# Optimization experiments

Hardware: AMD Instinct MI355X
Metric: run time of the kernel (lower is better)

## Reference

```python
import jax, jax.numpy as jnp
import numpy as np

B, T, H, S = 64, 512, 768, 128  # batch, seq_len, hidden_size, num_statements


def setup_inputs() -> dict:
    key = jax.random.key(0)
    ks = jax.random.split(key, 6)
    hidden = jax.random.normal(ks[0], (B, T, H), dtype=jnp.float32)
    # per-token statement ids, sorted (statements appear contiguously in source order)
    statements_ids = jnp.sort(jax.random.randint(ks[1], (B, T), 0, S), axis=-1).astype(jnp.int32)
    scale = 1.0 / np.sqrt(H)
    w1 = jax.random.normal(ks[2], (H, H), dtype=jnp.float32) * scale
    b1 = jnp.zeros((H,), dtype=jnp.float32)
    w2 = jax.random.normal(ks[3], (H, H), dtype=jnp.float32) * scale
    b2 = jnp.zeros((H,), dtype=jnp.float32)
    w3 = jax.random.normal(ks[4], (H, 1), dtype=jnp.float32) * scale
    b3 = jnp.zeros((1,), dtype=jnp.float32)
    return {"hidden": hidden, "statements_ids": statements_ids,
            "w1": w1, "b1": b1, "w2": w2, "b2": b2, "w3": w3, "b3": b3}


def _segment_mean(x, sid):
    # x: [T, H], sid: [T] -> [S, H] mean of tokens per statement id
    sums = jax.ops.segment_sum(x, sid, num_segments=S)            # [S, H]
    cnts = jax.ops.segment_sum(jnp.ones((x.shape[0],), x.dtype), sid, num_segments=S)  # [S]
    return sums / jnp.maximum(cnts, 1.0)[:, None]


def reference(hidden, statements_ids, w1, b1, w2, b2, w3, b3):
    # per-statement mean pooling (scatter-mean), vectorized over batch
    pooled = jax.vmap(_segment_mean)(hidden, statements_ids)      # [B, S, H]
    # CodeCoverageMLP: fc1 -> GELU -> fc2 -> GELU -> fc3 -> sigmoid (dropout = eval identity)
    x = jax.nn.gelu(pooled @ w1 + b1, approximate=False)
    x = jax.nn.gelu(x @ w2 + b2, approximate=False)
    preds = jax.nn.sigmoid(x @ w3 + b3)                           # [B, S, 1]
    return preds[..., 0]                                          # [B, S]
```

## Files before the change

### kernel.cpp

```cpp
#include <hip/hip_runtime.h>
#include <stdint.h>

#define NB 64
#define NT 512
#define NH 768
#define NS 128
#define NM (NB*NS)

typedef _Float16 half8 __attribute__((ext_vector_type(8)));
typedef _Float16 half4 __attribute__((ext_vector_type(4)));
typedef __attribute__((ext_vector_type(4))) float f32x4;

__device__ __forceinline__ float gelu_exact(float x) {
  return 0.5f * x * (1.0f + erff(x * 0.70710678118654752440f));
}

__device__ __forceinline__ void gll16(const void* g, void* l) {
  __builtin_amdgcn_global_load_lds(
      (__attribute__((address_space(1))) unsigned int*)g,
      (__attribute__((address_space(3))) unsigned int*)l,
      16, 0, 0);
}

__global__ void prep_w_kernel(const float* __restrict__ w1, const float* __restrict__ w2,
                              _Float16* __restrict__ W) {
  int id = blockIdx.x * 256 + threadIdx.x;
  int n  = id % NH;
  int t  = id / NH;
  int kc = t % 96;
  int w  = t / 96;
  const float* src = w ? w2 : w1;
  int k0 = kc * 8;
  half8 h;
#pragma unroll
  for (int i = 0; i < 8; ++i)
    h[i] = (_Float16)src[(size_t)(k0 + i) * NH + n];
  const size_t off = ((((size_t)w * 48 + (n >> 4)) * 96 + kc) * 16 + (n & 15)) * 8;
  *(half8*)&W[off] = h;
}

__global__ __launch_bounds__(256)
void pool_kernel(const float* __restrict__ hidden, const int* __restrict__ sid,
                 _Float16* __restrict__ Ahi, _Float16* __restrict__ Alo) {
  __shared__ int   s_sid[NT];
  __shared__ short s_e0[NS + 1];
  const int b = blockIdx.y, cc = blockIdx.x;
  const int tid = threadIdx.x;
  for (int t = tid; t < NT; t += 256) s_sid[t] = sid[b * NT + t];
  __syncthreads();
  for (int t = tid; t < NT; t += 256) {
    const int cur  = s_sid[t];
    const int prev = t ? s_sid[t - 1] : -1;
    for (int s = prev + 1; s <= cur; ++s) s_e0[s] = (short)t;
    if (t == NT - 1)
      for (int s = cur + 1; s <= NS; ++s) s_e0[s] = (short)NT;
  }
  __syncthreads();

  const int c4  = tid & 15;
  const int sg  = tid >> 4;
  const int col = cc * 64 + c4 * 4;
  const float* hb = hidden + (size_t)b * NT * NH;

  for (int s = sg; s < NS; s += 16) {
    const int e0 = s_e0[s], e1 = s_e0[s + 1];
    f32x4 acc = {0.f, 0.f, 0.f, 0.f};
    for (int t = e0; t < e1; ++t)
      acc += *(const f32x4*)(hb + (size_t)t * NH + col);
    const float inv = 1.0f / (float)((e1 > e0) ? (e1 - e0) : 1);
    const int m = b * NS + s;
    half4 h, l;
#pragma unroll
    for (int j = 0; j < 4; ++j) {
      float x = acc[j] * inv;
      h[j] = (_Float16)x;
      l[j] = (_Float16)(x - (float)h[j]);
    }
    const size_t off = (size_t)m * NH + col;
    *(half4*)&Ahi[off] = h;
    *(half4*)&Alo[off] = l;
  }
}

__global__ __launch_bounds__(512, 1)
void mlp_kernel(const _Float16* __restrict__ Ahi, const _Float16* __restrict__ Alo,
                const _Float16* __restrict__ Wp,
                const float* __restrict__ b1, const float* __restrict__ b2,
                const float* __restrict__ w3, const float* __restrict__ b3,
                float* __restrict__ out) {
  __shared__ _Float16 sA[2][2][4096];
  __shared__ _Float16 sX[32 * NH];
  __shared__ float    sP[8][32];

  const int tid  = threadIdx.x;
  const int lane = tid & 63;
  const int wv   = tid >> 6;
  const int lr   = lane & 15;
  const int lk4  = lane >> 4;
  const int row0 = blockIdx.x * 32;

  const _Float16* W1 = Wp;
  const _Float16* W2 = Wp + (size_t)NH * NH;

  const int   str  = wv * 4 + lk4;
  const int   scol = (lr * 8) ^ ((str & 7) << 3);
#define STAGE(b, kt) {                                                        \
    const size_t src = (size_t)(row0 + str) * NH + (kt) * 128 + scol;         \
    gll16(Ahi + src, &sA[b][0][wv * 512]);                                    \
    gll16(Alo + src, &sA[b][1][wv * 512]); }

  f32x4 acc1[2][6] = {};
  STAGE(0, 0);
  __syncthreads();
  for (int kt = 0; kt < 6; ++kt) {
    const int cur = kt & 1;
    if (kt < 5) STAGE(cur ^ 1, kt + 1);
#pragma unroll
    for (int kk = 0; kk < 4; ++kk) {
      half8 bw[6];
#pragma unroll
      for (int nf = 0; nf < 6; ++nf)
        bw[nf] = *(const half8*)(W1 + ((size_t)(wv * 6 + nf) * 96 + kt * 16 + kk * 4 + lk4) * 128 + lr * 8);
#pragma unroll
      for (int mf = 0; mf < 2; ++mf) {
        const int ar = mf * 16 + lr;
        const int ad = ar * 128 + ((kk * 32 + lk4 * 8) ^ ((ar & 7) << 3));
        half8 ah = *(const half8*)&sA[cur][0][ad];
        half8 al = *(const half8*)&sA[cur][1][ad];
#pragma unroll
        for (int nf = 0; nf < 6; ++nf) {
          acc1[mf][nf] = __builtin_amdgcn_mfma_f32_16x16x32_f16(ah, bw[nf], acc1[mf][nf], 0, 0, 0);
          acc1[mf][nf] = __builtin_amdgcn_mfma_f32_16x16x32_f16(al, bw[nf], acc1[mf][nf], 0, 0, 0);
        }
      }
    }
    __syncthreads();
  }

#pragma unroll
  for (int nf = 0; nf < 6; ++nf) {
    const int col = wv * 96 + nf * 16 + lr;
    const float bv = b1[col];
#pragma unroll
    for (int mf = 0; mf < 2; ++mf)
#pragma unroll
      for (int r = 0; r < 4; ++r) {
        const int row = mf * 16 + lk4 * 4 + r;
        sX[row * NH + (col ^ ((row & 7) << 3))] = (_Float16)gelu_exact(acc1[mf][nf][r] + bv);
      }
  }
  __syncthreads();

  f32x4 acc2[2][6] = {};
#pragma unroll 4
  for (int kb8 = 0; kb8 < 96; kb8 += 4) {
    half8 bw[6];
#pragma unroll
    for (int nf = 0; nf < 6; ++nf)
      bw[nf] = *(const half8*)(W2 + ((size_t)(wv * 6 + nf) * 96 + kb8 + lk4) * 128 + lr * 8);
#pragma unroll
    for (int mf = 0; mf < 2; ++mf) {
      const int ar = mf * 16 + lr;
      half8 a = *(const half8*)&sX[ar * NH + ((kb8 * 8 + lk4 * 8) ^ ((ar & 7) << 3))];
#pragma unroll
      for (int nf = 0; nf < 6; ++nf)
        acc2[mf][nf] = __builtin_amdgcn_mfma_f32_16x16x32_f16(a, bw[nf], acc2[mf][nf], 0, 0, 0);
    }
  }

  float p[2][4] = {};
#pragma unroll
  for (int nf = 0; nf < 6; ++nf) {
    const int col = wv * 96 + nf * 16 + lr;
    const float bv = b2[col], wvv = w3[col];
#pragma unroll
    for (int mf = 0; mf < 2; ++mf)
#pragma unroll
      for (int r = 0; r < 4; ++r)
        p[mf][r] += gelu_exact(acc2[mf][nf][r] + bv) * wvv;
  }
#pragma unroll
  for (int mf = 0; mf < 2; ++mf)
#pragma unroll
    for (int r = 0; r < 4; ++r) {
      float v = p[mf][r];
      v += __shfl_xor(v, 1, 16);
      v += __shfl_xor(v, 2, 16);
      v += __shfl_xor(v, 4, 16);
      v += __shfl_xor(v, 8, 16);
      if (lr == 0) sP[wv][mf * 16 + lk4 * 4 + r] = v;
    }
  __syncthreads();
  if (tid < 32) {
    float s = b3[0];
#pragma unroll
    for (int w = 0; w < 8; ++w) s += sP[w][tid];
    out[row0 + tid] = 1.0f / (1.0f + expf(-s));
  }
#undef STAGE
}

extern "C" void kernel_launch(void* const* d_in, const int* in_sizes, int n_in,
                              void* d_out, int out_size, void* d_ws, size_t ws_size,
                              hipStream_t stream) {
  (void)in_sizes; (void)n_in; (void)out_size; (void)ws_size;
  const float* hidden = (const float*)d_in[0];
  const int*   sid    = (const int*)d_in[1];
  const float* w1     = (const float*)d_in[2];
  const float* b1     = (const float*)d_in[3];
  const float* w2     = (const float*)d_in[4];
  const float* b2     = (const float*)d_in[5];
  const float* w3     = (const float*)d_in[6];
  const float* b3     = (const float*)d_in[7];
  float* out = (float*)d_out;

  char* p = (char*)d_ws;
  const size_t actE = (size_t)NM * NH;
  _Float16* Ahi = (_Float16*)p; p += actE * 2;
  _Float16* Alo = (_Float16*)p; p += actE * 2;
  _Float16* W   = (_Float16*)p; p += (size_t)2 * NH * NH * 2;

  prep_w_kernel<<<2 * 96 * NH / 256, 256, 0, stream>>>(w1, w2, W);
  pool_kernel<<<dim3(12, NB), 256, 0, stream>>>(hidden, sid, Ahi, Alo);
  mlp_kernel<<<NM / 32, 512, 0, stream>>>(Ahi, Alo, W, b1, b2, w3, b3, out);
}
```

Measured before the change: 235.2 us.

## Prefetch weight fragments in registers, single-buffer LDS, raise occupancy, fast GELU

Replaces exact erf-based GELU with an Abramowitz-Stegun polynomial approximation using hardware rcp and fast exp. The A tile in LDS goes from double to single buffer and sP aliases it, which shrinks shared memory. Launch bounds change from 1 to 4 blocks per SM so more blocks can reside at once. Weight fragments are software-prefetched one k-step ahead in registers in both GEMMs. The costs are an extra sync per k-tile that exposes staging latency, more register pressure from the prefetch buffers, and small accuracy loss in GELU.

```diff
diff --git a/kernel.cpp b/kernel.cpp
--- a/kernel.cpp
+++ b/kernel.cpp
@@ -11,8 +11,15 @@
 typedef _Float16 half4 __attribute__((ext_vector_type(4)));
 typedef __attribute__((ext_vector_type(4))) float f32x4;
 
-__device__ __forceinline__ float gelu_exact(float x) {
-  return 0.5f * x * (1.0f + erff(x * 0.70710678118654752440f));
+__device__ __forceinline__ float gelu_fast(float x) {
+  float ax = fabsf(x) * 0.70710678118654752440f;
+  float t  = __builtin_amdgcn_rcpf(1.0f + 0.3275911f * ax);
+  float e  = __expf(-ax * ax);
+  float poly = t * (0.254829592f + t * (-0.284496736f +
+               t * (1.421413741f + t * (-1.453152027f + t * 1.061405429f))));
+  float erfv = 1.0f - poly * e;
+  float phi  = 0.5f * (1.0f + copysignf(erfv, x));
+  return x * phi;
 }
 
 __device__ __forceinline__ void gll16(const void* g, void* l) {
@@ -82,15 +89,15 @@
   }
 }
 
-__global__ __launch_bounds__(512, 1)
+__global__ __launch_bounds__(512, 4)
 void mlp_kernel(const _Float16* __restrict__ Ahi, const _Float16* __restrict__ Alo,
                 const _Float16* __restrict__ Wp,
                 const float* __restrict__ b1, const float* __restrict__ b2,
                 const float* __restrict__ w3, const float* __restrict__ b3,
                 float* __restrict__ out) {
-  __shared__ _Float16 sA[2][2][4096];
+  __shared__ _Float16 sA[2][4096];
   __shared__ _Float16 sX[32 * NH];
-  __shared__ float    sP[8][32];
+  float (*sP)[32] = (float(*)[32])&sA[0][0];
 
   const int tid  = threadIdx.x;
   const int lane = tid & 63;
@@ -102,39 +109,48 @@
   const _Float16* W1 = Wp;
   const _Float16* W2 = Wp + (size_t)NH * NH;
 
-  const int   str  = wv * 4 + lk4;
-  const int   scol = (lr * 8) ^ ((str & 7) << 3);
-#define STAGE(b, kt) {                                                        \
+  const int str  = wv * 4 + lk4;
+  const int scol = (lr * 8) ^ ((str & 7) << 3);
+#define STAGE(kt) {                                                           \
     const size_t src = (size_t)(row0 + str) * NH + (kt) * 128 + scol;         \
-    gll16(Ahi + src, &sA[b][0][wv * 512]);                                    \
-    gll16(Alo + src, &sA[b][1][wv * 512]); }
+    gll16(Ahi + src, &sA[0][wv * 512]);                                       \
+    gll16(Alo + src, &sA[1][wv * 512]); }
 
   f32x4 acc1[2][6] = {};
-  STAGE(0, 0);
+  STAGE(0);
   __syncthreads();
   for (int kt = 0; kt < 6; ++kt) {
-    const int cur = kt & 1;
-    if (kt < 5) STAGE(cur ^ 1, kt + 1);
+    half8 bw[6], bwn[6];
+#pragma unroll
+    for (int nf = 0; nf < 6; ++nf)
+      bw[nf] = *(const half8*)(W1 + ((size_t)(wv * 6 + nf) * 96 + kt * 16 + lk4) * 128 + lr * 8);
 #pragma unroll
     for (int kk = 0; kk < 4; ++kk) {
-      half8 bw[6];
-#pragma unroll
-      for (int nf = 0; nf < 6; ++nf)
-        bw[nf] = *(const half8*)(W1 + ((size_t)(wv * 6 + nf) * 96 + kt * 16 + kk * 4 + lk4) * 128 + lr * 8);
+      if (kk < 3) {
+#pragma unroll
+        for (int nf = 0; nf < 6; ++nf)
+          bwn[nf] = *(const half8*)(W1 + ((size_t)(wv * 6 + nf) * 96 + kt * 16 + (kk + 1) * 4 + lk4) * 128 + lr * 8);
+      }
 #pragma unroll
       for (int mf = 0; mf < 2; ++mf) {
         const int ar = mf * 16 + lr;
         const int ad = ar * 128 + ((kk * 32 + lk4 * 8) ^ ((ar & 7) << 3));
-        half8 ah = *(const half8*)&sA[cur][0][ad];
-        half8 al = *(const half8*)&sA[cur][1][ad];
+        half8 ah = *(const half8*)&sA[0][ad];
+        half8 al = *(const half8*)&sA[1][ad];
 #pragma unroll
         for (int nf = 0; nf < 6; ++nf) {
           acc1[mf][nf] = __builtin_amdgcn_mfma_f32_16x16x32_f16(ah, bw[nf], acc1[mf][nf], 0, 0, 0);
           acc1[mf][nf] = __builtin_amdgcn_mfma_f32_16x16x32_f16(al, bw[nf], acc1[mf][nf], 0, 0, 0);
         }
       }
+#pragma unroll
+      for (int nf = 0; nf < 6; ++nf) bw[nf] = bwn[nf];
     }
     __syncthreads();
+    if (kt < 5) {
+      STAGE(kt + 1);
+      __syncthreads();
+    }
   }
 
 #pragma unroll
@@ -146,26 +162,33 @@
 #pragma unroll
       for (int r = 0; r < 4; ++r) {
         const int row = mf * 16 + lk4 * 4 + r;
-        sX[row * NH + (col ^ ((row & 7) << 3))] = (_Float16)gelu_exact(acc1[mf][nf][r] + bv);
+        sX[row * NH + (col ^ ((row & 7) << 3))] = (_Float16)gelu_fast(acc1[mf][nf][r] + bv);
       }
   }
   __syncthreads();
 
   f32x4 acc2[2][6] = {};
-#pragma unroll 4
-  for (int kb8 = 0; kb8 < 96; kb8 += 4) {
-    half8 bw[6];
-#pragma unroll
-    for (int nf = 0; nf < 6; ++nf)
-      bw[nf] = *(const half8*)(W2 + ((size_t)(wv * 6 + nf) * 96 + kb8 + lk4) * 128 + lr * 8);
+  half8 bw2[6], bw2n[6];
+#pragma unroll
+  for (int nf = 0; nf < 6; ++nf)
+    bw2[nf] = *(const half8*)(W2 + ((size_t)(wv * 6 + nf) * 96 + lk4) * 128 + lr * 8);
+  for (int g = 0; g < 24; ++g) {
+    if (g < 23) {
+#pragma unroll
+      for (int nf = 0; nf < 6; ++nf)
+        bw2n[nf] = *(const half8*)(W2 + ((size_t)(wv * 6 + nf) * 96 + (g + 1) * 4 + lk4) * 128 + lr * 8);
+    }
+    const int koff = g * 32 + lk4 * 8;
 #pragma unroll
     for (int mf = 0; mf < 2; ++mf) {
       const int ar = mf * 16 + lr;
-      half8 a = *(const half8*)&sX[ar * NH + ((kb8 * 8 + lk4 * 8) ^ ((ar & 7) << 3))];
+      half8 a = *(const half8*)&sX[ar * NH + (koff ^ ((ar & 7) << 3))];
 #pragma unroll
       for (int nf = 0; nf < 6; ++nf)
-        acc2[mf][nf] = __builtin_amdgcn_mfma_f32_16x16x32_f16(a, bw[nf], acc2[mf][nf], 0, 0, 0);
-    }
+        acc2[mf][nf] = __builtin_amdgcn_mfma_f32_16x16x32_f16(a, bw2[nf], acc2[mf][nf], 0, 0, 0);
+    }
+#pragma unroll
+    for (int nf = 0; nf < 6; ++nf) bw2[nf] = bw2n[nf];
   }
 
   float p[2][4] = {};
@@ -177,7 +200,7 @@
     for (int mf = 0; mf < 2; ++mf)
 #pragma unroll
       for (int r = 0; r < 4; ++r)
-        p[mf][r] += gelu_exact(acc2[mf][nf][r] + bv) * wvv;
+        p[mf][r] += gelu_fast(acc2[mf][nf][r] + bv) * wvv;
   }
 #pragma unroll
   for (int mf = 0; mf < 2; ++mf)
```

New measurement: 227.1 us. -3.5%, faster.
